# Kernel tuning notes

Measured on AMD Instinct MI355X. Metric: run time of the kernel, lower is better.

## Reference

```python
import jax, jax.numpy as jnp
import numpy as np

NUM_HEADS = 16
HEAD_DIM = 32  # dim=512 / num_heads=16


def _rel_pos_bias(table, index, window_area):
    # table: [(2W-1)^2, H], index: [N, N] int -> bias [1, H, N, N]
    bias = table[index.reshape(-1)].reshape(window_area, window_area, -1)
    return jnp.transpose(bias, (2, 0, 1))[None]


def setup_inputs() -> dict:
    key = jax.random.key(0)
    ks = jax.random.split(key, 6)
    B, N, C = 256, 196, 512
    x = jax.random.normal(ks[0], (B, N, C), dtype=jnp.float32)
    qkv_w = jax.random.normal(ks[1], (3 * C, C), dtype=jnp.float32) * 0.02
    proj_w = jax.random.normal(ks[2], (C, C), dtype=jnp.float32) * 0.02
    proj_b = jax.random.normal(ks[3], (C,), dtype=jnp.float32) * 0.02
    rel_pos_bias_table = jax.random.normal(ks[4], (729, NUM_HEADS), dtype=jnp.float32) * 0.02
    rel_pos_index = jax.random.randint(ks[5], (N, N), 0, 729, dtype=jnp.int64)
    return {
        "x": x,
        "qkv_w": qkv_w,
        "proj_w": proj_w,
        "proj_b": proj_b,
        "rel_pos_bias_table": rel_pos_bias_table,
        "rel_pos_index": rel_pos_index,
        "window_area": N,
    }


def reference(x, qkv_w, proj_w, proj_b, rel_pos_bias_table, rel_pos_index, window_area):
    B, N, C = x.shape
    H, hd = NUM_HEADS, HEAD_DIM
    scale = hd ** -0.5
    # qkv projection (no bias), split into q,k,v: [B, H, N, hd]
    qkv = (x @ qkv_w.T).reshape(B, N, 3, H, hd)
    qkv = jnp.transpose(qkv, (2, 0, 3, 1, 4))
    q, k, v = qkv[0], qkv[1], qkv[2]
    attn = jnp.einsum("bhnd,bhmd->bhnm", q * scale, k)
    attn = attn + _rel_pos_bias(rel_pos_bias_table, rel_pos_index, window_area)
    attn = jax.nn.softmax(attn, axis=-1)
    out = jnp.einsum("bhnm,bhmd->bhnd", attn, v)
    out = jnp.transpose(out, (0, 2, 1, 3)).reshape(B, N, C)
    return out @ proj_w.T + proj_b
```

## Files before the change

### kernel.cpp

```cpp
#include <hip/hip_runtime.h>
#include <hip/hip_bf16.h>


typedef unsigned short u16;
typedef unsigned int u32;
typedef __attribute__((ext_vector_type(8))) short bf16x8;
typedef __attribute__((ext_vector_type(4))) float f32x4;

__device__ __forceinline__ u16 f2bf(float f) {
  union { float f; unsigned u; } c; c.f = f;
  unsigned r = ((c.u >> 16) & 1u) + 0x7fffu;
  return (u16)((c.u + r) >> 16);
}

__global__ __launch_bounds__(256) void cvt_f32_bf16(const float* __restrict__ in,
                                                    u16* __restrict__ out, int n) {
  int i = (blockIdx.x * 256 + threadIdx.x) * 4;
  if (i >= n) return;
  float4 v = *(const float4*)(in + i);
  ushort4 o;
  o.x = f2bf(v.x); o.y = f2bf(v.y); o.z = f2bf(v.z); o.w = f2bf(v.w);
  *(ushort4*)(out + i) = o;
}

__global__ __launch_bounds__(256) void zero_vt_pad(u16* __restrict__ vt) {
  int i = blockIdx.x * 256 + threadIdx.x;
  if (i >= 4096 * 32 * 36) return;
  int row = i / 36, c = i - row * 36;
  vt[row * 232 + 196 + c] = 0;
}

__global__ __launch_bounds__(256) void build_bias(const float* __restrict__ table,
                                                  const int* __restrict__ idx,
                                                  u16* __restrict__ outb) {
  int e = blockIdx.x * 256 + threadIdx.x;
  int r = e & 3, lane = (e >> 2) & 63, rest = e >> 8;
  int mt = rest % 14; rest /= 14;
  int nt = rest % 13; int h = rest / 13;
  int n = nt * 16 + (lane & 15);
  int m = mt * 16 + ((lane >> 4) << 2) + r;
  float v;
  if (m < 196) {
    int nc = n < 196 ? n : 195;
    v = table[idx[nc * 196 + m] * 16 + h];
  } else {
    v = -1e30f;
  }
  outb[e] = f2bf(v);
}

template<int EPI>
__global__ __launch_bounds__(512, 2) void gemm256(
    const u16* __restrict__ A, const u16* __restrict__ Bt,
    u16* __restrict__ q, u16* __restrict__ kk, u16* __restrict__ vt,
    const float* __restrict__ pbias, float* __restrict__ out) {
  constexpr int K = 512;
  constexpr int NWGX = (EPI == 0) ? 6 : 2;
  constexpr int NWG = NWGX * 196;
  __shared__ __align__(16) u16 SMEM[65536];
  u16* LA = SMEM;
  u16* LB = SMEM + 32768;

  int id = blockIdx.y * NWGX + blockIdx.x;
  int nf = (id & 7) * (NWG >> 3) + (id >> 3);
  const int bx = nf / NWGX, by = nf - (nf / NWGX) * NWGX;

  const int tid = threadIdx.x;
  const int w = tid >> 6, l = tid & 63;
  const int lr = l & 15, lg = l >> 4;
  const int wm = w >> 2, wn = w & 3;

  const int gq = (l & 3) ^ ((l >> 3) & 3);
  const u16* gA = A + (long)(bx * 256 + w * 32 + (l >> 2)) * K + gq * 8;
  const u16* gB = Bt + (long)(by * 256 + w * 32 + (l >> 2)) * K + gq * 8;

  const int swz = (lg ^ ((lr >> 1) & 3)) * 8;
  const int ra = (wm * 128 + lr) * 32 + swz;
  const int rb = (wn * 64 + lr) * 32 + swz;

#define STAGE_A(st, kt)                                                        \
  __builtin_amdgcn_global_load_lds((const __attribute__((address_space(1))) void*)(gA + (kt) * 32), \
      (__attribute__((address_space(3))) void*)&LA[(st) * 8192 + w * 1024], 16, 0, 0); \
  __builtin_amdgcn_global_load_lds((const __attribute__((address_space(1))) void*)(gA + 16 * K + (kt) * 32), \
      (__attribute__((address_space(3))) void*)&LA[(st) * 8192 + w * 1024 + 512], 16, 0, 0);
#define STAGE_B(st, kt)                                                        \
  __builtin_amdgcn_global_load_lds((const __attribute__((address_space(1))) void*)(gB + (kt) * 32), \
      (__attribute__((address_space(3))) void*)&LB[(st) * 8192 + w * 1024], 16, 0, 0); \
  __builtin_amdgcn_global_load_lds((const __attribute__((address_space(1))) void*)(gB + 16 * K + (kt) * 32), \
      (__attribute__((address_space(3))) void*)&LB[(st) * 8192 + w * 1024 + 512], 16, 0, 0);

  f32x4 acc[8][4] = {};

  STAGE_A(0, 0); STAGE_B(0, 0);
  STAGE_A(1, 1); STAGE_B(1, 1);
  STAGE_A(2, 2); STAGE_B(2, 2);
  asm volatile("s_waitcnt vmcnt(8)" ::: "memory");
  __builtin_amdgcn_s_barrier();

  for (int kt = 0; kt < 16; ++kt) {
    const int slot = kt & 3;
    const int st = (kt + 3) & 3;
    const int sk = (kt + 3 < 16) ? kt + 3 : 15;
    const u16* as = &LA[slot * 8192];
    const u16* bs = &LB[slot * 8192];

    bf16x8 afr[8], bfr[4];
#pragma unroll
    for (int f = 0; f < 8; ++f) afr[f] = *(const bf16x8*)&as[ra + f * 512];
#pragma unroll
    for (int j2 = 0; j2 < 4; ++j2) bfr[j2] = *(const bf16x8*)&bs[rb + j2 * 512];
    STAGE_A(st, sk);
    STAGE_B(st, sk);
    asm volatile("s_waitcnt vmcnt(8)" ::: "memory");
    __builtin_amdgcn_s_barrier();
    asm volatile("s_waitcnt lgkmcnt(0)" ::: "memory");
    __builtin_amdgcn_s_setprio(1);
#pragma unroll
    for (int f = 0; f < 8; ++f)
#pragma unroll
      for (int j2 = 0; j2 < 4; ++j2)
        acc[f][j2] = __builtin_amdgcn_mfma_f32_16x16x32_bf16(afr[f], bfr[j2], acc[f][j2], 0, 0, 0);
    __builtin_amdgcn_s_setprio(0);
    __builtin_amdgcn_s_barrier();
  }
#undef STAGE_A
#undef STAGE_B
  asm volatile("s_waitcnt vmcnt(0)" ::: "memory");

  if (EPI == 0) {
    const int t = by >> 1;
    const int colbase = by * 256;
    const float s = (t == 0) ? 0.17677669529663687f : 1.0f;
#pragma unroll
    for (int p = 0; p < 2; ++p) {
      __syncthreads();
      if (wm == p) {
        if (t < 2) {
#pragma unroll
          for (int f = 0; f < 8; ++f)
#pragma unroll
            for (int j2 = 0; j2 < 4; ++j2)
#pragma unroll
              for (int r = 0; r < 4; ++r)
                SMEM[(f * 16 + lg * 4 + r) * 264 + wn * 64 + j2 * 16 + lr] =
                    f2bf(acc[f][j2][r] * s);
        } else {
#pragma unroll
          for (int f = 0; f < 8; ++f)
#pragma unroll
            for (int j2 = 0; j2 < 4; ++j2)
#pragma unroll
              for (int r = 0; r < 4; ++r)
                SMEM[(wn * 64 + j2 * 16 + lr) * 136 + f * 16 + lg * 4 + r] =
                    f2bf(acc[f][j2][r]);
        }
      }
      __syncthreads();
      const int growbase = bx * 256 + p * 128;
      if (t < 2) {
        u16* dst = (t == 0) ? q : kk;
        const int lrow = tid >> 2, ch = tid & 3;
        const int grow = growbase + lrow;
        const int bb2 = grow / 196, nn = grow - bb2 * 196;
#pragma unroll
        for (int i = 0; i < 8; ++i) {
          const int colle = (ch + i * 4) * 8;
          bf16x8 vv = *(const bf16x8*)&SMEM[lrow * 264 + colle];
          const int col = colbase + colle;
          const int h = (col >> 5) & 15, dd = col & 31;
          *(bf16x8*)&dst[((long)(bb2 * 16 + h) * 196 + nn) * 32 + dd] = vv;
        }
      } else {
        const int cl = tid >> 1, half = tid & 1;
        const int col = colbase + cl;
        const int h = (col >> 5) & 15, dd = col & 31;
#pragma unroll
        for (int i = 0; i < 8; ++i) {
          const int r0 = growbase + half * 64 + i * 8;
          bf16x8 vv = *(const bf16x8*)&SMEM[cl * 136 + half * 64 + i * 8];
          const int bb2 = r0 / 196, nn = r0 - bb2 * 196;
          if (nn + 8 <= 196) {
            *(bf16x8*)&vt[((long)(bb2 * 16 + h) * 32 + dd) * 232 + nn] = vv;
          } else {
#pragma unroll
            for (int e = 0; e < 8; ++e) {
              const int rr = r0 + e;
              const int b3 = rr / 196, n3 = rr - b3 * 196;
              vt[((long)(b3 * 16 + h) * 32 + dd) * 232 + n3] = (u16)((short*)&vv)[e];
            }
          }
        }
      }
    }
  } else {
    const int colbase = by * 256 + wn * 64;
    const int rowb = bx * 256 + wm * 128 + lg * 4;
#pragma unroll
    for (int f = 0; f < 8; ++f) {
      const int row0 = rowb + f * 16;
#pragma unroll
      for (int j2 = 0; j2 < 4; ++j2) {
        const int col = colbase + j2 * 16 + lr;
        const float pb = pbias[col];
#pragma unroll
        for (int r = 0; r < 4; ++r)
          out[(long)(row0 + r) * 512 + col] = acc[f][j2][r] + pb;
      }
    }
  }
}

__global__ __launch_bounds__(256, 4) void attn_kernel(
    const u16* __restrict__ q, const u16* __restrict__ kk,
    const u16* __restrict__ vt, const u16* __restrict__ biasA,
    u16* __restrict__ ao) {
  __shared__ u16 Ks[196 * 40];
  __shared__ u16 Vs[32 * 232];
  const int bhd = blockIdx.x;
  const int h = bhd >> 8, bb = bhd & 255;
  const int bh = bb * 16 + h;
  const int tid = threadIdx.x, w = tid >> 6, l = tid & 63;
  const int lr = l & 15, lg = l >> 4;

  {
    const u16* kg = kk + (long)bh * (196 * 32);
#pragma unroll
    for (int p = 0; p < 4; ++p) {
      int m = p * 64 + (tid >> 2);
      if (m < 196) {
        int c = (tid & 3) * 8;
        *(bf16x8*)&Ks[m * 40 + c] = *(const bf16x8*)(kg + m * 32 + c);
      }
    }
    const u16* vg = vt + (long)bh * (32 * 232);
#pragma unroll
    for (int p = 0; p < 4; ++p) {
      int off = (p * 256 + tid) * 8;
      if (off < 32 * 232) *(bf16x8*)&Vs[off] = *(const bf16x8*)(vg + off);
    }
  }
  __syncthreads();

  const u16* biasH = biasA + (long)h * (13 * 14 * 256);
  const int sA = ((l & 16) << 1) + lr;
  const int sB = sA + 16;
  const bool hi = (l & 32) != 0;

  for (int nt = w; nt < 13; nt += 4) {
    int nq = nt * 16 + lr; if (nq > 195) nq = 195;
    bf16x8 qa = *(const bf16x8*)(q + ((long)bh * 196 + nq) * 32 + lg * 8);

    u32 pk[14][2];
    float ssum = 0.f;
#pragma unroll
    for (int mt = 0; mt < 14; ++mt) {
      int row = mt * 16 + lr; if (row > 195) row = 195;
      bf16x8 kb = *(const bf16x8*)&Ks[row * 40 + lg * 8];
      const ushort4 b4 = *(const ushort4*)(biasH + ((nt * 14 + mt) * 64 + l) * 4);
      f32x4 c;
      c[0] = __uint_as_float(((u32)b4.x) << 16);
      c[1] = __uint_as_float(((u32)b4.y) << 16);
      c[2] = __uint_as_float(((u32)b4.z) << 16);
      c[3] = __uint_as_float(((u32)b4.w) << 16);
      f32x4 S = __builtin_amdgcn_mfma_f32_16x16x32_bf16(kb, qa, c, 0, 0, 0);
      float e0 = __expf(S[0]), e1 = __expf(S[1]);
      float e2 = __expf(S[2]), e3 = __expf(S[3]);
      ssum += (e0 + e1) + (e2 + e3);
      asm("v_cvt_pk_bf16_f32 %0, %1, %2" : "=v"(pk[mt][0]) : "v"(e0), "v"(e1));
      asm("v_cvt_pk_bf16_f32 %0, %1, %2" : "=v"(pk[mt][1]) : "v"(e2), "v"(e3));
    }
    ssum += __shfl_xor(ssum, 16);
    ssum += __shfl_xor(ssum, 32);
    float invT = __builtin_amdgcn_rcpf(ssum);

    f32x4 O0 = {}, O1 = {};
#pragma unroll
    for (int ks = 0; ks < 7; ++ks) {
      u32 a0 = (u32)__shfl((int)pk[2 * ks][0], sA);
      u32 a1 = (u32)__shfl((int)pk[2 * ks][1], sA);
      u32 a2 = (u32)__shfl((int)pk[2 * ks][0], sB);
      u32 a3 = (u32)__shfl((int)pk[2 * ks][1], sB);
      u32 c0 = (u32)__shfl((int)pk[2 * ks + 1][0], sA);
      u32 c1 = (u32)__shfl((int)pk[2 * ks + 1][1], sA);
      u32 c2 = (u32)__shfl((int)pk[2 * ks + 1][0], sB);
      u32 c3 = (u32)__shfl((int)pk[2 * ks + 1][1], sB);
      bf16x8 pa;
      ((u32*)&pa)[0] = hi ? c0 : a0;
      ((u32*)&pa)[1] = hi ? c1 : a1;
      ((u32*)&pa)[2] = hi ? c2 : a2;
      ((u32*)&pa)[3] = hi ? c3 : a3;
      bf16x8 v0 = *(const bf16x8*)&Vs[lr * 232 + ks * 32 + lg * 8];
      bf16x8 v1 = *(const bf16x8*)&Vs[(16 + lr) * 232 + ks * 32 + lg * 8];
      O0 = __builtin_amdgcn_mfma_f32_16x16x32_bf16(pa, v0, O0, 0, 0, 0);
      O1 = __builtin_amdgcn_mfma_f32_16x16x32_bf16(pa, v1, O1, 0, 0, 0);
    }

    float inv[4];
#pragma unroll
    for (int r = 0; r < 4; ++r) inv[r] = __shfl(invT, lg * 4 + r);
    const int nr0 = nt * 16 + lg * 4;
#pragma unroll
    for (int r = 0; r < 4; ++r) {
      int nr = nr0 + r;
      if (nr < 196) {
        long base = ((long)bb * 196 + nr) * 512 + h * 32;
        ao[base + lr] = f2bf(O0[r] * inv[r]);
        ao[base + 16 + lr] = f2bf(O1[r] * inv[r]);
      }
    }
  }
}

extern "C" void kernel_launch(void* const* d_in, const int* in_sizes, int n_in,
                              void* d_out, int out_size, void* d_ws, size_t ws_size,
                              hipStream_t stream) {
  const float* x      = (const float*)d_in[0];
  const float* qkv_w  = (const float*)d_in[1];
  const float* proj_w = (const float*)d_in[2];
  const float* proj_b = (const float*)d_in[3];
  const float* table  = (const float*)d_in[4];
  const int*   ridx   = (const int*)d_in[5];
  float* out = (float*)d_out;

  char* ws = (char*)d_ws;
  u16*   xb    = (u16*)(ws);
  u16*   qwb   = (u16*)(ws + 51380224);
  u16*   pwb   = (u16*)(ws + 52953088);
  u16*   qb    = (u16*)(ws + 53477376);
  u16*   kb    = (u16*)(ws + 104857600);
  u16*   vtb   = (u16*)(ws + 156237824);
  u16*   biasA = (u16*)(ws + 217055232);

  cvt_f32_bf16<<<25088, 256, 0, stream>>>(x, xb, 25690112);
  cvt_f32_bf16<<<768, 256, 0, stream>>>(qkv_w, qwb, 786432);
  cvt_f32_bf16<<<256, 256, 0, stream>>>(proj_w, pwb, 262144);
  build_bias<<<2912, 256, 0, stream>>>(table, ridx, biasA);
  zero_vt_pad<<<18432, 256, 0, stream>>>(vtb);

  gemm256<0><<<dim3(6, 196), 512, 0, stream>>>(xb, qwb, qb, kb, vtb, nullptr, nullptr);
  attn_kernel<<<4096, 256, 0, stream>>>(qb, kb, vtb, biasA, xb );
  gemm256<1><<<dim3(2, 196), 512, 0, stream>>>(xb, pwb, nullptr, nullptr, nullptr, proj_b, out);
}
```

Before: 280.5 us.

## Restructure GEMM mainloop into 8-phase double-buffered ping-pong schedule

Replaces the 4-slot, 16-iteration K-loop of both projection GEMMs with a fully unrolled 8-tile, double-buffered schedule. Each K-tile of 64 is split into four MFMA phases that interleave LDS fragment reads, global-to-LDS prefetches and barriers. The aim is finer-grained overlap of memory loads with MFMA work and less register pressure per phase (4 A fragments instead of 8). In exchange there are many more barriers per tile, and the waitcnt accounting becomes harder to reason about.

```diff
diff --git a/kernel.cpp b/kernel.cpp
--- a/kernel.cpp
+++ b/kernel.cpp
@@ -6,6 +6,9 @@
 typedef unsigned int u32;
 typedef __attribute__((ext_vector_type(8))) short bf16x8;
 typedef __attribute__((ext_vector_type(4))) float f32x4;
+
+#define AS1 __attribute__((address_space(1)))
+#define AS3 __attribute__((address_space(3)))
 
 __device__ __forceinline__ u16 f2bf(float f) {
   union { float f; unsigned u; } c; c.f = f;
@@ -49,17 +52,76 @@
   outb[e] = f2bf(v);
 }
 
+template<int KT>
+__device__ __forceinline__ void ktile(u16* __restrict__ SMEM,
+    const u16* __restrict__ gA0, const u16* __restrict__ gA1,
+    const u16* __restrict__ gB0, const u16* __restrict__ gB1,
+    int wbase, int rdA, int rdB, f32x4 (&acc)[8][4]) {
+  constexpr int BUF = KT & 1, OBUF = BUF ^ 1;
+  constexpr bool STG = (KT < 7);
+  constexpr int C = (KT + 1) * 64;
+  bf16x8 afr[4], bfr[4];
+
+#define LOADPAIR(dst, g0, g1, coloff)                                          \
+  __builtin_amdgcn_global_load_lds((const AS1 void*)((g0) + (coloff)),         \
+      (AS3 void*)&SMEM[(dst) + wbase], 16, 0, 0);                              \
+  __builtin_amdgcn_global_load_lds((const AS1 void*)((g1) + (coloff)),         \
+      (AS3 void*)&SMEM[(dst) + 4096 + wbase], 16, 0, 0);
+#define MFMA16(FH)                                                             \
+  __builtin_amdgcn_s_setprio(1);                                               \
+  _Pragma("unroll") for (int q = 0; q < 4; ++q)                                \
+    _Pragma("unroll") for (int j = 0; j < 4; ++j)                              \
+      acc[(FH)*4 + q][j] = __builtin_amdgcn_mfma_f32_16x16x32_bf16(            \
+          afr[q], bfr[j], acc[(FH)*4 + q][j], 0, 0, 0);                        \
+  __builtin_amdgcn_s_setprio(0);
+
+#pragma unroll
+  for (int j = 0; j < 4; ++j) bfr[j] = *(const bf16x8*)&SMEM[rdB + BUF * 16384 + j * 512];
+#pragma unroll
+  for (int q = 0; q < 4; ++q) afr[q] = *(const bf16x8*)&SMEM[rdA + BUF * 16384 + q * 512];
+  if constexpr (STG) { LOADPAIR(OBUF * 16384, gA0, gA1, C) }
+  __builtin_amdgcn_s_barrier();
+  asm volatile("s_waitcnt lgkmcnt(0)" ::: "memory");
+  MFMA16(0)
+  __builtin_amdgcn_s_barrier();
+#pragma unroll
+  for (int q = 0; q < 4; ++q) afr[q] = *(const bf16x8*)&SMEM[rdA + BUF * 16384 + (q + 4) * 512];
+  if constexpr (STG) { LOADPAIR(32768 + OBUF * 16384, gB0, gB1, C) }
+  __builtin_amdgcn_s_barrier();
+  asm volatile("s_waitcnt lgkmcnt(0)" ::: "memory");
+  MFMA16(1)
+  if constexpr (STG) { asm volatile("s_waitcnt vmcnt(4)" ::: "memory"); }
+  else               { asm volatile("s_waitcnt vmcnt(0)" ::: "memory"); }
+  __builtin_amdgcn_s_barrier();
+#pragma unroll
+  for (int j = 0; j < 4; ++j) bfr[j] = *(const bf16x8*)&SMEM[rdB + BUF * 16384 + 8192 + j * 512];
+#pragma unroll
+  for (int q = 0; q < 4; ++q) afr[q] = *(const bf16x8*)&SMEM[rdA + BUF * 16384 + 8192 + q * 512];
+  if constexpr (STG) { LOADPAIR(OBUF * 16384 + 8192, gA0, gA1, C + 32) }
+  __builtin_amdgcn_s_barrier();
+  asm volatile("s_waitcnt lgkmcnt(0)" ::: "memory");
+  MFMA16(0)
+  __builtin_amdgcn_s_barrier();
+#pragma unroll
+  for (int q = 0; q < 4; ++q) afr[q] = *(const bf16x8*)&SMEM[rdA + BUF * 16384 + 8192 + (q + 4) * 512];
+  if constexpr (STG) { LOADPAIR(32768 + OBUF * 16384 + 8192, gB0, gB1, C + 32) }
+  __builtin_amdgcn_s_barrier();
+  asm volatile("s_waitcnt lgkmcnt(0)" ::: "memory");
+  MFMA16(1)
+  if constexpr (STG) { asm volatile("s_waitcnt vmcnt(4)" ::: "memory"); }
+  __builtin_amdgcn_s_barrier();
+#undef LOADPAIR
+#undef MFMA16
+}
+
 template<int EPI>
-__global__ __launch_bounds__(512, 2) void gemm256(
+__global__ __launch_bounds__(512, 2) void gemm8p(
     const u16* __restrict__ A, const u16* __restrict__ Bt,
     u16* __restrict__ q, u16* __restrict__ kk, u16* __restrict__ vt,
     const float* __restrict__ pbias, float* __restrict__ out) {
-  constexpr int K = 512;
   constexpr int NWGX = (EPI == 0) ? 6 : 2;
   constexpr int NWG = NWGX * 196;
   __shared__ __align__(16) u16 SMEM[65536];
-  u16* LA = SMEM;
-  u16* LB = SMEM + 32768;
 
   int id = blockIdx.y * NWGX + blockIdx.x;
   int nf = (id & 7) * (NWG >> 3) + (id >> 3);
@@ -70,62 +132,43 @@
   const int lr = l & 15, lg = l >> 4;
   const int wm = w >> 2, wn = w & 3;
 
-  const int gq = (l & 3) ^ ((l >> 3) & 3);
-  const u16* gA = A + (long)(bx * 256 + w * 32 + (l >> 2)) * K + gq * 8;
-  const u16* gB = Bt + (long)(by * 256 + w * 32 + (l >> 2)) * K + gq * 8;
-
-  const int swz = (lg ^ ((lr >> 1) & 3)) * 8;
-  const int ra = (wm * 128 + lr) * 32 + swz;
-  const int rb = (wn * 64 + lr) * 32 + swz;
-
-#define STAGE_A(st, kt)                                                        \
-  __builtin_amdgcn_global_load_lds((const __attribute__((address_space(1))) void*)(gA + (kt) * 32), \
-      (__attribute__((address_space(3))) void*)&LA[(st) * 8192 + w * 1024], 16, 0, 0); \
-  __builtin_amdgcn_global_load_lds((const __attribute__((address_space(1))) void*)(gA + 16 * K + (kt) * 32), \
-      (__attribute__((address_space(3))) void*)&LA[(st) * 8192 + w * 1024 + 512], 16, 0, 0);
-#define STAGE_B(st, kt)                                                        \
-  __builtin_amdgcn_global_load_lds((const __attribute__((address_space(1))) void*)(gB + (kt) * 32), \
-      (__attribute__((address_space(3))) void*)&LB[(st) * 8192 + w * 1024], 16, 0, 0); \
-  __builtin_amdgcn_global_load_lds((const __attribute__((address_space(1))) void*)(gB + 16 * K + (kt) * 32), \
-      (__attribute__((address_space(3))) void*)&LB[(st) * 8192 + w * 1024 + 512], 16, 0, 0);
+  const int gsw = (l & 3) ^ ((l >> 3) & 3);
+  const u16* gA0 = A + (size_t)(bx * 256 + w * 16 + (l >> 2)) * 512 + gsw * 8;
+  const u16* gA1 = gA0 + 65536;
+  const u16* gB0 = Bt + (size_t)(by * 256 + w * 16 + (l >> 2)) * 512 + gsw * 8;
+  const u16* gB1 = gB0 + 65536;
+  const int wbase = w * 512;
+
+  const int rsw = (lg ^ ((lr >> 1) & 3)) * 8;
+  const int rdA = (wm * 128 + lr) * 32 + rsw;
+  const int rdB = 32768 + (wn * 64 + lr) * 32 + rsw;
 
   f32x4 acc[8][4] = {};
 
-  STAGE_A(0, 0); STAGE_B(0, 0);
-  STAGE_A(1, 1); STAGE_B(1, 1);
-  STAGE_A(2, 2); STAGE_B(2, 2);
-  asm volatile("s_waitcnt vmcnt(8)" ::: "memory");
-  __builtin_amdgcn_s_barrier();
-
-  for (int kt = 0; kt < 16; ++kt) {
-    const int slot = kt & 3;
-    const int st = (kt + 3) & 3;
-    const int sk = (kt + 3 < 16) ? kt + 3 : 15;
-    const u16* as = &LA[slot * 8192];
-    const u16* bs = &LB[slot * 8192];
-
-    bf16x8 afr[8], bfr[4];
-#pragma unroll
-    for (int f = 0; f < 8; ++f) afr[f] = *(const bf16x8*)&as[ra + f * 512];
-#pragma unroll
-    for (int j2 = 0; j2 < 4; ++j2) bfr[j2] = *(const bf16x8*)&bs[rb + j2 * 512];
-    STAGE_A(st, sk);
-    STAGE_B(st, sk);
-    asm volatile("s_waitcnt vmcnt(8)" ::: "memory");
-    __builtin_amdgcn_s_barrier();
-    asm volatile("s_waitcnt lgkmcnt(0)" ::: "memory");
-    __builtin_amdgcn_s_setprio(1);
-#pragma unroll
-    for (int f = 0; f < 8; ++f)
-#pragma unroll
-      for (int j2 = 0; j2 < 4; ++j2)
-        acc[f][j2] = __builtin_amdgcn_mfma_f32_16x16x32_bf16(afr[f], bfr[j2], acc[f][j2], 0, 0, 0);
-    __builtin_amdgcn_s_setprio(0);
-    __builtin_amdgcn_s_barrier();
-  }
-#undef STAGE_A
-#undef STAGE_B
-  asm volatile("s_waitcnt vmcnt(0)" ::: "memory");
+#define PLP(dst, g0, g1, coloff)                                               \
+  __builtin_amdgcn_global_load_lds((const AS1 void*)((g0) + (coloff)),         \
+      (AS3 void*)&SMEM[(dst) + wbase], 16, 0, 0);                              \
+  __builtin_amdgcn_global_load_lds((const AS1 void*)((g1) + (coloff)),         \
+      (AS3 void*)&SMEM[(dst) + 4096 + wbase], 16, 0, 0);
+  PLP(0, gA0, gA1, 0)
+  asm volatile("" ::: "memory");
+  PLP(32768, gB0, gB1, 0)
+  asm volatile("" ::: "memory");
+  PLP(8192, gA0, gA1, 32)
+  asm volatile("" ::: "memory");
+  PLP(32768 + 8192, gB0, gB1, 32)
+#undef PLP
+  asm volatile("s_waitcnt vmcnt(4)" ::: "memory");
+  __builtin_amdgcn_s_barrier();
+
+  ktile<0>(SMEM, gA0, gA1, gB0, gB1, wbase, rdA, rdB, acc);
+  ktile<1>(SMEM, gA0, gA1, gB0, gB1, wbase, rdA, rdB, acc);
+  ktile<2>(SMEM, gA0, gA1, gB0, gB1, wbase, rdA, rdB, acc);
+  ktile<3>(SMEM, gA0, gA1, gB0, gB1, wbase, rdA, rdB, acc);
+  ktile<4>(SMEM, gA0, gA1, gB0, gB1, wbase, rdA, rdB, acc);
+  ktile<5>(SMEM, gA0, gA1, gB0, gB1, wbase, rdA, rdB, acc);
+  ktile<6>(SMEM, gA0, gA1, gB0, gB1, wbase, rdA, rdB, acc);
+  ktile<7>(SMEM, gA0, gA1, gB0, gB1, wbase, rdA, rdB, acc);
 
   if (EPI == 0) {
     const int t = by >> 1;
@@ -137,22 +180,22 @@
       if (wm == p) {
         if (t < 2) {
 #pragma unroll
-          for (int f = 0; f < 8; ++f)
-#pragma unroll
-            for (int j2 = 0; j2 < 4; ++j2)
-#pragma unroll
-              for (int r = 0; r < 4; ++r)
-                SMEM[(f * 16 + lg * 4 + r) * 264 + wn * 64 + j2 * 16 + lr] =
-                    f2bf(acc[f][j2][r] * s);
+        for (int f = 0; f < 8; ++f)
+#pragma unroll
+          for (int j2 = 0; j2 < 4; ++j2)
+#pragma unroll
+            for (int r = 0; r < 4; ++r)
+              SMEM[(f * 16 + lg * 4 + r) * 264 + wn * 64 + j2 * 16 + lr] =
+                  f2bf(acc[f][j2][r] * s);
         } else {
 #pragma unroll
-          for (int f = 0; f < 8; ++f)
-#pragma unroll
-            for (int j2 = 0; j2 < 4; ++j2)
-#pragma unroll
-              for (int r = 0; r < 4; ++r)
-                SMEM[(wn * 64 + j2 * 16 + lr) * 136 + f * 16 + lg * 4 + r] =
-                    f2bf(acc[f][j2][r]);
+        for (int f = 0; f < 8; ++f)
+#pragma unroll
+          for (int j2 = 0; j2 < 4; ++j2)
+#pragma unroll
+            for (int r = 0; r < 4; ++r)
+              SMEM[(wn * 64 + j2 * 16 + lr) * 136 + f * 16 + lg * 4 + r] =
+                  f2bf(acc[f][j2][r]);
         }
       }
       __syncthreads();
@@ -168,7 +211,7 @@
           bf16x8 vv = *(const bf16x8*)&SMEM[lrow * 264 + colle];
           const int col = colbase + colle;
           const int h = (col >> 5) & 15, dd = col & 31;
-          *(bf16x8*)&dst[((long)(bb2 * 16 + h) * 196 + nn) * 32 + dd] = vv;
+          *(bf16x8*)&dst[((size_t)(bb2 * 16 + h) * 196 + nn) * 32 + dd] = vv;
         }
       } else {
         const int cl = tid >> 1, half = tid & 1;
@@ -180,13 +223,13 @@
           bf16x8 vv = *(const bf16x8*)&SMEM[cl * 136 + half * 64 + i * 8];
           const int bb2 = r0 / 196, nn = r0 - bb2 * 196;
           if (nn + 8 <= 196) {
-            *(bf16x8*)&vt[((long)(bb2 * 16 + h) * 32 + dd) * 232 + nn] = vv;
+            *(bf16x8*)&vt[((size_t)(bb2 * 16 + h) * 32 + dd) * 232 + nn] = vv;
           } else {
 #pragma unroll
             for (int e = 0; e < 8; ++e) {
               const int rr = r0 + e;
               const int b3 = rr / 196, n3 = rr - b3 * 196;
-              vt[((long)(b3 * 16 + h) * 32 + dd) * 232 + n3] = (u16)((short*)&vv)[e];
+              vt[((size_t)(b3 * 16 + h) * 32 + dd) * 232 + n3] = (u16)((short*)&vv)[e];
             }
           }
         }
@@ -204,7 +247,7 @@
         const float pb = pbias[col];
 #pragma unroll
         for (int r = 0; r < 4; ++r)
-          out[(long)(row0 + r) * 512 + col] = acc[f][j2][r] + pb;
+          out[(size_t)(row0 + r) * 512 + col] = acc[f][j2][r] + pb;
       }
     }
   }
@@ -223,7 +266,7 @@
   const int lr = l & 15, lg = l >> 4;
 
   {
-    const u16* kg = kk + (long)bh * (196 * 32);
+    const u16* kg = kk + (size_t)bh * (196 * 32);
 #pragma unroll
     for (int p = 0; p < 4; ++p) {
       int m = p * 64 + (tid >> 2);
@@ -232,7 +275,7 @@
         *(bf16x8*)&Ks[m * 40 + c] = *(const bf16x8*)(kg + m * 32 + c);
       }
     }
-    const u16* vg = vt + (long)bh * (32 * 232);
+    const u16* vg = vt + (size_t)bh * (32 * 232);
 #pragma unroll
     for (int p = 0; p < 4; ++p) {
       int off = (p * 256 + tid) * 8;
@@ -241,14 +284,14 @@
   }
   __syncthreads();
 
-  const u16* biasH = biasA + (long)h * (13 * 14 * 256);
+  const u16* biasH = biasA + (size_t)h * (13 * 14 * 256);
   const int sA = ((l & 16) << 1) + lr;
   const int sB = sA + 16;
   const bool hi = (l & 32) != 0;
 
   for (int nt = w; nt < 13; nt += 4) {
     int nq = nt * 16 + lr; if (nq > 195) nq = 195;
-    bf16x8 qa = *(const bf16x8*)(q + ((long)bh * 196 + nq) * 32 + lg * 8);
+    bf16x8 qa = *(const bf16x8*)(q + ((size_t)bh * 196 + nq) * 32 + lg * 8);
 
     u32 pk[14][2];
     float ssum = 0.f;
@@ -303,7 +346,7 @@
     for (int r = 0; r < 4; ++r) {
       int nr = nr0 + r;
       if (nr < 196) {
-        long base = ((long)bb * 196 + nr) * 512 + h * 32;
+        size_t base = ((size_t)bb * 196 + nr) * 512 + h * 32;
         ao[base + lr] = f2bf(O0[r] * inv[r]);
         ao[base + 16 + lr] = f2bf(O1[r] * inv[r]);
       }
@@ -337,7 +380,7 @@
   build_bias<<<2912, 256, 0, stream>>>(table, ridx, biasA);
   zero_vt_pad<<<18432, 256, 0, stream>>>(vtb);
 
-  gemm256<0><<<dim3(6, 196), 512, 0, stream>>>(xb, qwb, qb, kb, vtb, nullptr, nullptr);
+  gemm8p<0><<<dim3(6, 196), 512, 0, stream>>>(xb, qwb, qb, kb, vtb, nullptr, nullptr);
   attn_kernel<<<4096, 256, 0, stream>>>(qb, kb, vtb, biasA, xb );
-  gemm256<1><<<dim3(2, 196), 512, 0, stream>>>(xb, pwb, nullptr, nullptr, nullptr, proj_b, out);
-}
+  gemm8p<1><<<dim3(2, 196), 512, 0, stream>>>(xb, pwb, nullptr, nullptr, nullptr, proj_b, out);
+}
```

Result: faster. 273.7 us (-2.4%).
